# Performance work log

Hardware: AMD Instinct MI355X
Metric: run time of the kernel (lower is better)

Reference implementation:

```python
import jax, jax.numpy as jnp
import numpy as np

BIG = 1e10  # sentinel for masked-out (padded) points, like pytorch3d's masking


def setup_inputs() -> dict:
    key = jax.random.key(0)
    k1, k2, k3, k4 = jax.random.split(key, 4)
    B, N, M = 16, 4096, 4096
    source_cloud = jax.random.normal(k1, (B, N, 2), dtype=jnp.float32)
    target_cloud = jax.random.normal(k2, (B, M, 2), dtype=jnp.float32)
    source_mask = jax.random.randint(k3, (B,), 0, N)  # lengths1
    target_mask = jax.random.randint(k4, (B,), 0, M)  # lengths2
    return {
        "source_cloud": source_cloud,
        "target_cloud": target_cloud,
        "source_mask": source_mask,
        "target_mask": target_mask,
    }


def reference(source_cloud, target_cloud, source_mask, target_mask):
    # source_cloud: [B, N, 2], target_cloud: [B, M, 2]
    # source_mask/target_mask: int lengths [B] (knn_points lengths1/lengths2)
    B, N, _ = source_cloud.shape
    M = target_cloud.shape[1]

    s2 = jnp.sum(source_cloud * source_cloud, axis=-1)  # [B, N]
    t2 = jnp.sum(target_cloud * target_cloud, axis=-1)  # [B, M]
    # squared pairwise distances [B, N, M]
    d2 = (s2[:, :, None] + t2[:, None, :]
          - 2.0 * jnp.einsum('bnd,bmd->bnm', source_cloud, target_cloud))

    src_valid = jnp.arange(N)[None, :] < source_mask[:, None]  # [B, N]
    tgt_valid = jnp.arange(M)[None, :] < target_mask[:, None]  # [B, M]

    # forward: for each source point, 1-NN over valid target points
    d2_fwd = jnp.where(tgt_valid[:, None, :], d2, BIG)
    min_fwd = jnp.maximum(jnp.min(d2_fwd, axis=-1), 0.0)  # [B, N]
    # backward: for each target point, 1-NN over valid source points
    d2_bwd = jnp.where(src_valid[:, :, None], d2, BIG)
    min_bwd = jnp.maximum(jnp.min(d2_bwd, axis=-2), 0.0)  # [B, M]

    # padded query points get dist 0 (pytorch3d knn_points semantics), then sqrt
    chamfer_forward = jnp.where(src_valid, jnp.sqrt(min_fwd), 0.0)
    chamfer_backward = jnp.where(tgt_valid, jnp.sqrt(min_bwd), 0.0)
    return (chamfer_forward, chamfer_backward)
```

## Files before the change

### kernel.cpp

```cpp
#include <hip/hip_runtime.h>


#define NQ 16
typedef float f2 __attribute__((ext_vector_type(2)));

template<int KA>
__device__ __forceinline__ void scan_queries(
    const float* __restrict__ Qrow,
    const float4* __restrict__ sxy, const f2* __restrict__ sn,
    unsigned* __restrict__ orow_u, int tid)
{
    float mx[KA], my[KA], s2[KA], best[KA];
    #pragma unroll
    for (int k = 0; k < KA; ++k) {
        const float2 q = ((const float2*)Qrow)[tid + k * 256];
        mx[k] = -2.f * q.x;
        my[k] = -2.f * q.y;
        s2[k] = fmaf(q.x, q.x, q.y * q.y);
        best[k] = 3.0e38f;
    }

    #pragma unroll 4
    for (int j = 0; j < 64; ++j) {
        const float4 xy = sxy[j];
        const f2 xp = f2{xy.x, xy.y};
        const f2 yp = f2{xy.z, xy.w};
        const f2 np = sn[j];
        #pragma unroll
        for (int k = 0; k < KA; ++k) {
            f2 v = xp * mx[k] + np;
            v = yp * my[k] + v;
            best[k] = fminf(best[k], fminf(v.x, v.y));
        }
    }

    #pragma unroll
    for (int k = 0; k < KA; ++k) {
        const float d = sqrtf(fmaxf(best[k] + s2[k], 0.f));
        atomicMin(orow_u + tid + k * 256, __float_as_uint(d));
    }
}

__global__ __launch_bounds__(256, 2) void chamfer_main(
    const float* __restrict__ src, const float* __restrict__ tgt,
    const int* __restrict__ slen, const int* __restrict__ tlen,
    float* __restrict__ out)
{
    __shared__ float4 sh_xy[64];
    __shared__ f2     sh_n[64];

    const int g   = blockIdx.x;
    const int tid = threadIdx.x;

    int row = -1, pc = 0, Lp = 0, acc = 0;
    #pragma unroll
    for (int rr = 0; rr < 32; ++rr) {
        const int L = (rr < 16) ? tlen[rr] : slen[rr - 16];
        const int n = (L + 127) >> 7;
        if (row < 0 && g < acc + n) { row = rr; pc = g - acc; Lp = L; }
        acc += n;
    }

    if (row < 0) {
        const int cr = g - acc;
        if (cr < 32) {
            const int dirc = cr >> 4, bc = cr & 15;
            const int Lpc = dirc ? slen[bc] : tlen[bc];
            if (Lpc == 0) {
                const int Lqc = dirc ? tlen[bc] : slen[bc];
                unsigned* op = (unsigned*)(out + cr * 4096);
                const unsigned sent = __float_as_uint(sqrtf(1e10f));
                #pragma unroll
                for (int k = 0; k < 16; ++k) {
                    const int q = tid + k * 256;
                    atomicMin(op + q, (q < Lqc) ? sent : 0u);
                }
            }
        }
        return;
    }
    const int dir = row >> 4, b = row & 15;

    const int Lq = dir ? tlen[b] : slen[b];
    unsigned* orow_u = (unsigned*)(out + row * 4096);

    if (pc == 0) {
        #pragma unroll
        for (int k = 0; k < 16; ++k) {
            const int q = tid + k * 256;
            if (q >= Lq) atomicMin(orow_u + q, 0u);
        }
    }

    const int KACT = (Lq + 255) >> 8;
    if (KACT == 0) return;

    const float* Q = dir ? tgt : src;
    const float* P = dir ? src : tgt;

    if (tid < 64) {
        const int base = pc * 128 + tid * 2;
        const float4 pp = ((const float4*)P)[(b * 4096 + base) >> 1];
        const float n0 = (base + 0 < Lp) ? fmaf(pp.x, pp.x, pp.y * pp.y) : 1e30f;
        const float n1 = (base + 1 < Lp) ? fmaf(pp.z, pp.z, pp.w * pp.w) : 1e30f;
        sh_xy[tid] = make_float4(pp.x, pp.z, pp.y, pp.w);
        sh_n[tid]  = f2{n0, n1};
    }
    __syncthreads();

    const float* Qrow = Q + b * 8192;

    switch ((KACT + 3) >> 2) {
        case 1:  scan_queries< 4>(Qrow, sh_xy, sh_n, orow_u, tid); break;
        case 2:  scan_queries< 8>(Qrow, sh_xy, sh_n, orow_u, tid); break;
        case 3:  scan_queries<12>(Qrow, sh_xy, sh_n, orow_u, tid); break;
        default: scan_queries<16>(Qrow, sh_xy, sh_n, orow_u, tid); break;
    }
}

extern "C" void kernel_launch(void* const* d_in, const int* in_sizes, int n_in,
                              void* d_out, int out_size, void* d_ws, size_t ws_size,
                              hipStream_t stream) {
    const float* src = (const float*)d_in[0];
    const float* tgt = (const float*)d_in[1];
    const int* slen  = (const int*)d_in[2];
    const int* tlen  = (const int*)d_in[3];
    (void)d_ws; (void)ws_size;

    hipMemsetAsync(d_out, 0x7F, (size_t)out_size * sizeof(float), stream);
    chamfer_main<<<1024, 256, 0, stream>>>(src, tgt, slen, tlen, (float*)d_out);
}
```

Measured before the change: 79.28 us.

## Use 512-thread blocks with fixed grid mapping and 256-point target chunks

Changes the work decomposition from a length-dependent packed grid of 1024 blocks × 256 threads (128-point chunks, up to 16 queries per thread) to a fixed 512-block grid of 512 threads. Each block handles a 256-point chunk with up to 8 queries per thread, and blocks whose chunk lies beyond the valid length exit early. This removes the per-block prefix scan over lengths and halves the number of atomicMin writes per query. The cost is that idle blocks are launched for short clouds and each block carries more threads, which changes register pressure and occupancy.

Measured after the change: 90.94 us. 14.7% more time.

```diff
diff --git a/kernel.cpp b/kernel.cpp
--- a/kernel.cpp
+++ b/kernel.cpp
@@ -1,7 +1,6 @@
 #include <hip/hip_runtime.h>
 
 
-#define NQ 16
 typedef float f2 __attribute__((ext_vector_type(2)));
 
 template<int KA>
@@ -13,7 +12,7 @@
     float mx[KA], my[KA], s2[KA], best[KA];
     #pragma unroll
     for (int k = 0; k < KA; ++k) {
-        const float2 q = ((const float2*)Qrow)[tid + k * 256];
+        const float2 q = ((const float2*)Qrow)[tid + k * 512];
         mx[k] = -2.f * q.x;
         my[k] = -2.f * q.y;
         s2[k] = fmaf(q.x, q.x, q.y * q.y);
@@ -21,7 +20,7 @@
     }
 
     #pragma unroll 4
-    for (int j = 0; j < 64; ++j) {
+    for (int j = 0; j < 128; ++j) {
         const float4 xy = sxy[j];
         const f2 xp = f2{xy.x, xy.y};
         const f2 yp = f2{xy.z, xy.w};
@@ -37,69 +36,57 @@
     #pragma unroll
     for (int k = 0; k < KA; ++k) {
         const float d = sqrtf(fmaxf(best[k] + s2[k], 0.f));
-        atomicMin(orow_u + tid + k * 256, __float_as_uint(d));
+        atomicMin(orow_u + tid + k * 512, __float_as_uint(d));
     }
 }
 
-__global__ __launch_bounds__(256, 2) void chamfer_main(
+__global__ __launch_bounds__(512, 2) void chamfer_main(
     const float* __restrict__ src, const float* __restrict__ tgt,
     const int* __restrict__ slen, const int* __restrict__ tlen,
     float* __restrict__ out)
 {
-    __shared__ float4 sh_xy[64];
-    __shared__ f2     sh_n[64];
+    __shared__ float4 sh_xy[128];
+    __shared__ f2     sh_n[128];
 
     const int g   = blockIdx.x;
     const int tid = threadIdx.x;
+    const int row = g & 31;
+    const int pc  = g >> 5;
+    const int dir = row >> 4, b = row & 15;
 
-    int row = -1, pc = 0, Lp = 0, acc = 0;
-    #pragma unroll
-    for (int rr = 0; rr < 32; ++rr) {
-        const int L = (rr < 16) ? tlen[rr] : slen[rr - 16];
-        const int n = (L + 127) >> 7;
-        if (row < 0 && g < acc + n) { row = rr; pc = g - acc; Lp = L; }
-        acc += n;
-    }
+    const int Lq = dir ? tlen[b] : slen[b];
+    const int Lp = dir ? slen[b] : tlen[b];
+    unsigned* orow_u = (unsigned*)(out + row * 4096);
 
-    if (row < 0) {
-        const int cr = g - acc;
-        if (cr < 32) {
-            const int dirc = cr >> 4, bc = cr & 15;
-            const int Lpc = dirc ? slen[bc] : tlen[bc];
-            if (Lpc == 0) {
-                const int Lqc = dirc ? tlen[bc] : slen[bc];
-                unsigned* op = (unsigned*)(out + cr * 4096);
-                const unsigned sent = __float_as_uint(sqrtf(1e10f));
-                #pragma unroll
-                for (int k = 0; k < 16; ++k) {
-                    const int q = tid + k * 256;
-                    atomicMin(op + q, (q < Lqc) ? sent : 0u);
-                }
+    if (Lp == 0) {
+        if (pc == 0) {
+            const unsigned sent = __float_as_uint(sqrtf(1e10f));
+            #pragma unroll
+            for (int k = 0; k < 8; ++k) {
+                const int q = tid + k * 512;
+                atomicMin(orow_u + q, (q < Lq) ? sent : 0u);
             }
         }
         return;
     }
-    const int dir = row >> 4, b = row & 15;
-
-    const int Lq = dir ? tlen[b] : slen[b];
-    unsigned* orow_u = (unsigned*)(out + row * 4096);
+    if (pc * 256 >= Lp) return;
 
     if (pc == 0) {
         #pragma unroll
-        for (int k = 0; k < 16; ++k) {
-            const int q = tid + k * 256;
+        for (int k = 0; k < 8; ++k) {
+            const int q = tid + k * 512;
             if (q >= Lq) atomicMin(orow_u + q, 0u);
         }
     }
 
-    const int KACT = (Lq + 255) >> 8;
+    const int KACT = (Lq + 511) >> 9;
     if (KACT == 0) return;
 
     const float* Q = dir ? tgt : src;
     const float* P = dir ? src : tgt;
 
-    if (tid < 64) {
-        const int base = pc * 128 + tid * 2;
+    if (tid < 128) {
+        const int base = pc * 256 + tid * 2;
         const float4 pp = ((const float4*)P)[(b * 4096 + base) >> 1];
         const float n0 = (base + 0 < Lp) ? fmaf(pp.x, pp.x, pp.y * pp.y) : 1e30f;
         const float n1 = (base + 1 < Lp) ? fmaf(pp.z, pp.z, pp.w * pp.w) : 1e30f;
@@ -110,11 +97,11 @@
 
     const float* Qrow = Q + b * 8192;
 
-    switch ((KACT + 3) >> 2) {
-        case 1:  scan_queries< 4>(Qrow, sh_xy, sh_n, orow_u, tid); break;
-        case 2:  scan_queries< 8>(Qrow, sh_xy, sh_n, orow_u, tid); break;
-        case 3:  scan_queries<12>(Qrow, sh_xy, sh_n, orow_u, tid); break;
-        default: scan_queries<16>(Qrow, sh_xy, sh_n, orow_u, tid); break;
+    switch ((KACT + 1) >> 1) {
+        case 1:  scan_queries<2>(Qrow, sh_xy, sh_n, orow_u, tid); break;
+        case 2:  scan_queries<4>(Qrow, sh_xy, sh_n, orow_u, tid); break;
+        case 3:  scan_queries<6>(Qrow, sh_xy, sh_n, orow_u, tid); break;
+        default: scan_queries<8>(Qrow, sh_xy, sh_n, orow_u, tid); break;
     }
 }
 
@@ -128,5 +115,5 @@
     (void)d_ws; (void)ws_size;
 
     hipMemsetAsync(d_out, 0x7F, (size_t)out_size * sizeof(float), stream);
-    chamfer_main<<<1024, 256, 0, stream>>>(src, tgt, slen, tlen, (float*)d_out);
+    chamfer_main<<<512, 512, 0, stream>>>(src, tgt, slen, tlen, (float*)d_out);
 }
```

## Split query rows into 1024-query groups per block and filter atomics

Applied to the files above, without the earlier changes.

Each block now handles one 128-point chunk paired with one group of up to 1024 queries instead of all queries. The grid grows to 4096 blocks and launch bounds rise to 4 blocks per CU, which gives finer load balance and more parallelism. Before each atomicMin the kernel reads the current output value and skips the atomic when the new value cannot improve it, cutting atomic traffic. The cost is that each block re-reads the shared chunk, runs a more expensive block-to-work mapping with a division, and carries fewer accumulators per thread.

New measurement: 78.15 us, median of 2. No clear change (-1.4%).

```diff
diff --git a/kernel.cpp b/kernel.cpp
--- a/kernel.cpp
+++ b/kernel.cpp
@@ -1,19 +1,18 @@
 #include <hip/hip_runtime.h>
 
 
-#define NQ 16
 typedef float f2 __attribute__((ext_vector_type(2)));
 
 template<int KA>
 __device__ __forceinline__ void scan_queries(
     const float* __restrict__ Qrow,
     const float4* __restrict__ sxy, const f2* __restrict__ sn,
-    unsigned* __restrict__ orow_u, int tid)
+    unsigned* __restrict__ orow_u, int tid, int q0)
 {
     float mx[KA], my[KA], s2[KA], best[KA];
     #pragma unroll
     for (int k = 0; k < KA; ++k) {
-        const float2 q = ((const float2*)Qrow)[tid + k * 256];
+        const float2 q = ((const float2*)Qrow)[q0 + tid + k * 256];
         mx[k] = -2.f * q.x;
         my[k] = -2.f * q.y;
         s2[k] = fmaf(q.x, q.x, q.y * q.y);
@@ -34,14 +33,20 @@
         }
     }
 
+    unsigned cur[KA];
+    #pragma unroll
+    for (int k = 0; k < KA; ++k)
+        cur[k] = orow_u[q0 + tid + k * 256];
     #pragma unroll
     for (int k = 0; k < KA; ++k) {
         const float d = sqrtf(fmaxf(best[k] + s2[k], 0.f));
-        atomicMin(orow_u + tid + k * 256, __float_as_uint(d));
+        const unsigned bits = __float_as_uint(d);
+        if (bits < cur[k])
+            atomicMin(orow_u + q0 + tid + k * 256, bits);
     }
 }
 
-__global__ __launch_bounds__(256, 2) void chamfer_main(
+__global__ __launch_bounds__(256, 4) void chamfer_main(
     const float* __restrict__ src, const float* __restrict__ tgt,
     const int* __restrict__ slen, const int* __restrict__ tlen,
     float* __restrict__ out)
@@ -52,13 +57,22 @@
     const int g   = blockIdx.x;
     const int tid = threadIdx.x;
 
-    int row = -1, pc = 0, Lp = 0, acc = 0;
+    int row = -1, pc = 0, qg = 0, Lp = 0, Lq = 0, acc = 0;
     #pragma unroll
     for (int rr = 0; rr < 32; ++rr) {
-        const int L = (rr < 16) ? tlen[rr] : slen[rr - 16];
-        const int n = (L + 127) >> 7;
-        if (row < 0 && g < acc + n) { row = rr; pc = g - acc; Lp = L; }
-        acc += n;
+        const int Ls  = (rr < 16) ? tlen[rr] : slen[rr - 16];
+        const int Lqq = (rr < 16) ? slen[rr] : tlen[rr - 16];
+        const int nch  = (Ls + 127) >> 7;
+        const int kact = (Lqq + 255) >> 8;
+        int nqg = (kact + 3) >> 2;
+        if (nqg == 0) nqg = 1;
+        const int units = nch * nqg;
+        if (row < 0 && g < acc + units) {
+            row = rr; const int u = g - acc;
+            pc = u / nqg; qg = u - pc * nqg;
+            Lp = Ls; Lq = Lqq;
+        }
+        acc += units;
     }
 
     if (row < 0) {
@@ -80,11 +94,9 @@
         return;
     }
     const int dir = row >> 4, b = row & 15;
-
-    const int Lq = dir ? tlen[b] : slen[b];
     unsigned* orow_u = (unsigned*)(out + row * 4096);
 
-    if (pc == 0) {
+    if (pc == 0 && qg == 0) {
         #pragma unroll
         for (int k = 0; k < 16; ++k) {
             const int q = tid + k * 256;
@@ -93,7 +105,8 @@
     }
 
     const int KACT = (Lq + 255) >> 8;
-    if (KACT == 0) return;
+    const int KB = min(4, KACT - qg * 4);
+    if (KB <= 0) return;
 
     const float* Q = dir ? tgt : src;
     const float* P = dir ? src : tgt;
@@ -109,12 +122,13 @@
     __syncthreads();
 
     const float* Qrow = Q + b * 8192;
+    const int q0 = qg * 1024;
 
-    switch ((KACT + 3) >> 2) {
-        case 1:  scan_queries< 4>(Qrow, sh_xy, sh_n, orow_u, tid); break;
-        case 2:  scan_queries< 8>(Qrow, sh_xy, sh_n, orow_u, tid); break;
-        case 3:  scan_queries<12>(Qrow, sh_xy, sh_n, orow_u, tid); break;
-        default: scan_queries<16>(Qrow, sh_xy, sh_n, orow_u, tid); break;
+    switch (KB) {
+        case 1:  scan_queries<1>(Qrow, sh_xy, sh_n, orow_u, tid, q0); break;
+        case 2:  scan_queries<2>(Qrow, sh_xy, sh_n, orow_u, tid, q0); break;
+        case 3:  scan_queries<3>(Qrow, sh_xy, sh_n, orow_u, tid, q0); break;
+        default: scan_queries<4>(Qrow, sh_xy, sh_n, orow_u, tid, q0); break;
     }
 }
 
@@ -128,5 +142,5 @@
     (void)d_ws; (void)ws_size;
 
     hipMemsetAsync(d_out, 0x7F, (size_t)out_size * sizeof(float), stream);
-    chamfer_main<<<1024, 256, 0, stream>>>(src, tgt, slen, tlen, (float*)d_out);
+    chamfer_main<<<4096, 256, 0, stream>>>(src, tgt, slen, tlen, (float*)d_out);
 }
```
